# Optimization experiments

Measured on AMD Instinct MI355X. Metric: run time of the kernel, lower is better.

## Reference

```python
import jax, jax.numpy as jnp
import numpy as np

K = 22                       # structuring element is 22x22 ones
ORIGIN = K // 2              # kornia origin = k//2 -> pad (11 before, 10 after)
PAD = ((0, 0), (0, 0), (ORIGIN, K - ORIGIN - 1), (ORIGIN, K - ORIGIN - 1))
WIN = (1, 1, K, K)
STRIDES = (1, 1, 1, 1)


def _erode(x):
    # flat (all-ones) structuring element erosion == sliding-window min.
    # Padding with +inf matches kornia's 'pad with max_val' for erosion.
    return jax.lax.reduce_window(x, float('inf'), jax.lax.min, WIN, STRIDES, PAD)


def _dilate(x):
    # flat dilation == sliding-window max; pad with -inf (kornia pads -max_val).
    return jax.lax.reduce_window(x, float('-inf'), jax.lax.max, WIN, STRIDES, PAD)


def setup_inputs() -> dict:
    key = jax.random.key(0)
    image = jax.random.uniform(key, (8, 3, 1024, 1024), dtype=jnp.float32)
    return {"image": image}


def reference(image):
    # morphological opening = erosion followed by dilation (same kernel)
    return _dilate(_erode(image))
```

## Files before the change

kernel.cpp:

```cpp
#include <hip/hip_runtime.h>


#define HH 1024
#define WW 1024
#define KW 22
#define SB 116
#define PINF __builtin_inff()

template<bool IS_MIN>
__device__ __forceinline__ float vop(float a, float b) {
    return IS_MIN ? fminf(a, b) : fmaxf(a, b);
}

template<bool IS_MIN, int COUT, class Get, class Put>
__device__ __forceinline__ void vanherk(Get get, Put put) {
    constexpr int NIN = COUT + KW - 1;
    constexpr int NB = (NIN + KW - 1) / KW;
    const float ID = IS_MIN ? PINF : -PINF;
    float Sprev[KW];
    #pragma unroll
    for (int j = 0; j < NB; ++j) {
        const int base = KW * j;
        const int needed = (NIN - base) < KW ? (NIN - base) : KW;
        float v[KW];
        #pragma unroll
        for (int m = 0; m < KW; ++m)
            if (m < needed) v[m] = get(base + m);
        float p = ID;
        #pragma unroll
        for (int m = 0; m < KW; ++m) {
            if (m < needed) {
                p = vop<IS_MIN>(p, v[m]);
                const int k = base - (KW - 1) + m;
                if (k >= 0 && k < COUT) {
                    if (m == KW - 1) put(k, p);
                    else             put(k, vop<IS_MIN>(Sprev[m + 1], p));
                }
            }
        }
        if (j < NB - 1) {
            float s = ID;
            #pragma unroll
            for (int m = KW - 1; m >= 0; --m) {
                s = vop<IS_MIN>(s, v[m]);
                Sprev[m] = s;
            }
        }
    }
}

template<bool INTERIOR>
__device__ __forceinline__ void tile_body(const float* __restrict__ src,
                                          float* __restrict__ dst,
                                          int R, int C, float* B, int t) {
    if (t < 216) {
        const int ch = t >= 108;
        const int j = ch ? t - 108 : t;
        const int base_o = ch ? 43 : 0;
        int cj = C - 22 + j;
        bool colOK = true;
        if (!INTERIOR) {
            colOK = (unsigned)cj < WW;
            cj = cj < 0 ? 0 : (cj > WW - 1 ? WW - 1 : cj);
        }
        const float* col = src + cj;
        const int rbase = R - 22 + base_o;
        vanherk<true, 43>(
            [&](int p) {
                int r = rbase + p;
                if (INTERIOR) return col[r * WW];
                int rc = r < 0 ? 0 : (r > HH - 1 ? HH - 1 : r);
                float vv = col[rc * WW];
                return (colOK && (unsigned)r < HH) ? vv : PINF;
            },
            [&](int k, float vv) { B[(base_o + k) * SB + j] = vv; });
    }
    __syncthreads();

    if (t < 170) {
        const int o = t >> 1;
        const int half = t & 1;
        float* Brow = B + o * SB;

        const int e0 = half * 44;
        float in1[68];
        {
            const float4* Br = (const float4*)(Brow + e0);
            #pragma unroll
            for (int i = 0; i < 17; ++i) {
                float4 x = Br[i];
                in1[4 * i] = x.x; in1[4 * i + 1] = x.y;
                in1[4 * i + 2] = x.z; in1[4 * i + 3] = x.w;
            }
        }
        float er[44];
        vanherk<true, 44>(
            [&](int p) { return in1[p]; },
            [&](int k, float vv) { er[k] = vv; });
        if (!INTERIOR) {
            const bool rOK = (unsigned)(R - 11 + o) < HH;
            #pragma unroll
            for (int k = 0; k < 44; ++k) {
                const int cimg = C - 11 + e0 + k;
                if (!rOK || (unsigned)cimg >= WW) er[k] = -PINF;
            }
        }
        __threadfence_block();
        {
            float4* Bw = (float4*)(Brow + e0);
            #pragma unroll
            for (int i = 0; i < 11; ++i)
                Bw[i] = make_float4(er[4 * i], er[4 * i + 1],
                                    er[4 * i + 2], er[4 * i + 3]);
        }
        __threadfence_block();

        const int c0 = half * 32;
        float in2[56];
        {
            const float4* Br = (const float4*)(Brow + c0);
            #pragma unroll
            for (int i = 0; i < 14; ++i) {
                float4 x = Br[i];
                in2[4 * i] = x.x; in2[4 * i + 1] = x.y;
                in2[4 * i + 2] = x.z; in2[4 * i + 3] = x.w;
            }
        }
        float rx[32];
        vanherk<false, 32>(
            [&](int p) { return in2[p]; },
            [&](int k, float vv) { rx[k] = vv; });
        __threadfence_block();
        {
            float4* Bw = (float4*)(Brow + c0);
            #pragma unroll
            for (int i = 0; i < 8; ++i)
                Bw[i] = make_float4(rx[4 * i], rx[4 * i + 1],
                                    rx[4 * i + 2], rx[4 * i + 3]);
        }
    }
    __syncthreads();

    if (t >= 128) {
        const int tt = t - 128;
        const int c = tt & 63;
        const int y0 = (tt >> 6) << 5;
        float o32[32];
        vanherk<false, 32>(
            [&](int p) { return B[(y0 + p) * SB + c]; },
            [&](int k, float vv) { o32[k] = vv; });
        #pragma unroll
        for (int k = 0; k < 32; ++k)
            dst[(R + y0 + k) * WW + C + c] = o32[k];
    }
}

__global__ __launch_bounds__(256, 4) void fused_open(const float* __restrict__ in,
                                                     float* __restrict__ out) {
    __shared__ float B[86 * SB];
    const int t = threadIdx.x;
    const int b = blockIdx.x;
    const int plane = b >> 8;
    const int by = (b >> 4) & 15;
    const int bx = b & 15;
    const int R = by * 64, C = bx * 64;
    const float* src = in + (size_t)plane * (HH * WW);
    float* dst = out + (size_t)plane * (HH * WW);

    if (by >= 1 && by <= 14 && bx >= 1 && bx <= 14)
        tile_body<true>(src, dst, R, C, B, t);
    else
        tile_body<false>(src, dst, R, C, B, t);
}

extern "C" void kernel_launch(void* const* d_in, const int* in_sizes, int n_in,
                              void* d_out, int out_size, void* d_ws, size_t ws_size,
                              hipStream_t stream) {
    const float* in = (const float*)d_in[0];
    float* out = (float*)d_out;
    (void)d_ws; (void)ws_size;
    fused_open<<<24 * 16 * 16, 256, 0, stream>>>(in, out);
}
```

Before: 187.2 us.

## Rebalance work across all 256 threads in each morphology stage

Redistributes the per-stage work so all four wavefronts participate: column pass split by wavefront slot, horizontal erosion/dilation split into three chunks per row over 255 threads, and final vertical dilation split into four 16-row groups. The per-row intra-thread fences are replaced with block-wide barriers, since threads now overlap neighbouring chunks of the same row. This aims to reduce load imbalance and idle wavefronts, at the cost of more redundant van Herk overlap work and extra __syncthreads.

```diff
diff --git a/kernel.cpp b/kernel.cpp
--- a/kernel.cpp
+++ b/kernel.cpp
@@ -53,10 +53,12 @@
 __device__ __forceinline__ void tile_body(const float* __restrict__ src,
                                           float* __restrict__ dst,
                                           int R, int C, float* B, int t) {
-    if (t < 216) {
-        const int ch = t >= 108;
-        const int j = ch ? t - 108 : t;
-        const int base_o = ch ? 43 : 0;
+    const int w = t >> 6, slot = t & 63;
+
+    if (slot < 54) {
+        const int ch = w >> 1;
+        const int j = (w & 1) * 54 + slot;
+        const int base_o = ch * 43;
         int cj = C - 22 + j;
         bool colOK = true;
         if (!INTERIOR) {
@@ -77,81 +79,88 @@
     }
     __syncthreads();
 
-    if (t < 170) {
-        const int o = t >> 1;
-        const int half = t & 1;
+    {
+        const bool act = t < 255;
+        const int ch = (3 * t + 2) >> 8;
+        const int o = t - 85 * ch;
+        const int g0 = 7 * ch;
         float* Brow = B + o * SB;
-
-        const int e0 = half * 44;
-        float in1[68];
-        {
-            const float4* Br = (const float4*)(Brow + e0);
+        float in1[56];
+        if (act) {
             #pragma unroll
-            for (int i = 0; i < 17; ++i) {
-                float4 x = Br[i];
+            for (int i = 0; i < 14; ++i) {
+                float4 x = ((const float4*)Brow)[g0 + i];
                 in1[4 * i] = x.x; in1[4 * i + 1] = x.y;
                 in1[4 * i + 2] = x.z; in1[4 * i + 3] = x.w;
             }
         }
-        float er[44];
-        vanherk<true, 44>(
-            [&](int p) { return in1[p]; },
-            [&](int k, float vv) { er[k] = vv; });
-        if (!INTERIOR) {
-            const bool rOK = (unsigned)(R - 11 + o) < HH;
-            #pragma unroll
-            for (int k = 0; k < 44; ++k) {
-                const int cimg = C - 11 + e0 + k;
-                if (!rOK || (unsigned)cimg >= WW) er[k] = -PINF;
+        float er[32];
+        if (act) {
+            vanherk<true, 32>(
+                [&](int p) { return in1[p]; },
+                [&](int k, float vv) { er[k] = vv; });
+            if (!INTERIOR) {
+                const bool rOK = (unsigned)(R - 11 + o) < HH;
+                #pragma unroll
+                for (int k = 0; k < 32; ++k) {
+                    const int cimg = C - 11 + 28 * ch + k;
+                    if (!rOK || (unsigned)cimg >= WW) er[k] = -PINF;
+                }
             }
         }
-        __threadfence_block();
-        {
-            float4* Bw = (float4*)(Brow + e0);
+        __syncthreads();
+        if (act) {
             #pragma unroll
-            for (int i = 0; i < 11; ++i)
-                Bw[i] = make_float4(er[4 * i], er[4 * i + 1],
-                                    er[4 * i + 2], er[4 * i + 3]);
+            for (int i = 0; i < 8; ++i)
+                ((float4*)Brow)[g0 + i] =
+                    make_float4(er[4 * i], er[4 * i + 1],
+                                er[4 * i + 2], er[4 * i + 3]);
         }
-        __threadfence_block();
+        __syncthreads();
+    }
 
-        const int c0 = half * 32;
-        float in2[56];
-        {
-            const float4* Br = (const float4*)(Brow + c0);
+    {
+        const bool act = t < 255;
+        const int ch = (3 * t + 2) >> 8;
+        const int o = t - 85 * ch;
+        const int g0 = 5 * ch;
+        float* Brow = B + o * SB;
+        float in2[48];
+        if (act) {
             #pragma unroll
-            for (int i = 0; i < 14; ++i) {
-                float4 x = Br[i];
+            for (int i = 0; i < 12; ++i) {
+                float4 x = ((const float4*)Brow)[g0 + i];
                 in2[4 * i] = x.x; in2[4 * i + 1] = x.y;
                 in2[4 * i + 2] = x.z; in2[4 * i + 3] = x.w;
             }
         }
-        float rx[32];
-        vanherk<false, 32>(
-            [&](int p) { return in2[p]; },
-            [&](int k, float vv) { rx[k] = vv; });
-        __threadfence_block();
-        {
-            float4* Bw = (float4*)(Brow + c0);
+        float rx[24];
+        if (act) {
+            vanherk<false, 24>(
+                [&](int p) { return in2[p]; },
+                [&](int k, float vv) { rx[k] = vv; });
+        }
+        __syncthreads();
+        if (act) {
             #pragma unroll
-            for (int i = 0; i < 8; ++i)
-                Bw[i] = make_float4(rx[4 * i], rx[4 * i + 1],
-                                    rx[4 * i + 2], rx[4 * i + 3]);
+            for (int i = 0; i < 6; ++i)
+                ((float4*)Brow)[g0 + i] =
+                    make_float4(rx[4 * i], rx[4 * i + 1],
+                                rx[4 * i + 2], rx[4 * i + 3]);
         }
+        __syncthreads();
     }
-    __syncthreads();
 
-    if (t >= 128) {
-        const int tt = t - 128;
-        const int c = tt & 63;
-        const int y0 = (tt >> 6) << 5;
-        float o32[32];
-        vanherk<false, 32>(
+    {
+        const int c = t & 63;
+        const int y0 = (t >> 6) << 4;
+        float o16[16];
+        vanherk<false, 16>(
             [&](int p) { return B[(y0 + p) * SB + c]; },
-            [&](int k, float vv) { o32[k] = vv; });
+            [&](int k, float vv) { o16[k] = vv; });
         #pragma unroll
-        for (int k = 0; k < 32; ++k)
-            dst[(R + y0 + k) * WW + C + c] = o32[k];
+        for (int k = 0; k < 16; ++k)
+            dst[(R + y0 + k) * WW + C + c] = o16[k];
     }
 }
 
```

Result: no change. 184.4 us (-1.5%).
